# Kernel tuning notes

Measured on AMD Instinct MI355X. Metric: run time of the kernel, lower is better.

Reference implementation:

```python
import jax, jax.numpy as jnp
import numpy as np

N_NODES = 20000
NEG_SLOPE = 0.2
EPS = 1e-10


def _gat_reparam_layer(x, W, att_i, att_j, bias, src, dst, heads, c2):
    """GATConv (PyG-style, aggr='add') whose output encodes (mean, std) per head,
    followed by diag-Gaussian reparameterization with N(0,1) prior (eval mode:
    output = mean; ixz = KL(q||p) summed over channels, averaged over heads).
    x: [N, F]; W: [F, heads*c2]; att_i/att_j: [heads, c2]; bias: [heads*c2].
    c2 = 2 * out_channels (mean + std logits).
    Returns out [N, heads*(c2//2)], ixz [N]."""
    N = x.shape[0]
    h = (x @ W).reshape(N, heads, c2)                      # [N, H, 2C]
    h_i = h[dst]                                           # [E, H, 2C] target (x_i)
    h_j = h[src]                                           # [E, H, 2C] source (x_j)
    # attention logits: leaky_relu((x_i*att_i).sum + (x_j*att_j).sum)
    logits = jnp.sum(h_i * att_i, axis=-1) + jnp.sum(h_j * att_j, axis=-1)  # [E, H]
    logits = jax.nn.leaky_relu(logits, NEG_SLOPE)
    # segment softmax over incoming edges of each target node
    lmax = jax.ops.segment_max(logits, dst, num_segments=N)  # [N, H]
    ex = jnp.exp(logits - lmax[dst])                         # [E, H]
    denom = jax.ops.segment_sum(ex, dst, num_segments=N)     # [N, H]
    alpha = ex / denom[dst]                                  # [E, H]
    # weighted scatter-add aggregation
    msg = alpha[:, :, None] * h_j                            # [E, H, 2C]
    out = jax.ops.segment_sum(msg, dst, num_segments=N)      # [N, H, 2C]
    out = out + bias.reshape(1, heads, c2)
    # reparameterization: split per head into mean / std
    C = c2 // 2
    mean = out[..., :C]                                      # [N, H, C]
    std = jax.nn.softplus(out[..., C:]) + EPS                # [N, H, C]
    # KL(N(mean, std) || N(0, 1)) per element, sum over C, mean over heads
    kl = 0.5 * (std * std + mean * mean - 1.0) - jnp.log(std)
    ixz = kl.sum(-1).mean(-1)                                # [N]
    return mean.reshape(N, heads * C), ixz


def setup_inputs() -> dict:
    key = jax.random.key(0)
    ks = jax.random.split(key, 10)
    N, F1 = N_NODES, 256
    E = 320000
    H1, C1 = 8, 32    # conv1: latent_size//2 = 32 per head, doubled for (mean,std)
    H2, C2 = 1, 16    # conv2: num_classes = 16
    edge_index = jax.random.randint(ks[0], (2, E), 0, N, dtype=jnp.int32)
    s = 0.1
    return {
        "x": jax.random.normal(ks[1], (N, F1), jnp.float32),
        "edge_index": edge_index,
        "W1": jax.random.normal(ks[2], (F1, H1 * 2 * C1), jnp.float32) * s,
        "att_i1": jax.random.normal(ks[3], (H1, 2 * C1), jnp.float32) * s,
        "att_j1": jax.random.normal(ks[4], (H1, 2 * C1), jnp.float32) * s,
        "bias1": jax.random.normal(ks[5], (H1 * 2 * C1,), jnp.float32) * s,
        "W2": jax.random.normal(ks[6], (H1 * C1, H2 * 2 * C2), jnp.float32) * s,
        "att_i2": jax.random.normal(ks[7], (H2, 2 * C2), jnp.float32) * s,
        "att_j2": jax.random.normal(ks[8], (H2, 2 * C2), jnp.float32) * s,
        "bias2": jax.random.normal(ks[9], (H2 * 2 * C2,), jnp.float32) * s,
    }


def reference(x, edge_index, W1, att_i1, att_j1, bias1, W2, att_i2, att_j2, bias2):
    src, dst = edge_index[0], edge_index[1]
    # eval mode: dropout is identity, output = posterior mean (val_use_mean=True)
    h1, ixz1 = _gat_reparam_layer(x, W1, att_i1, att_j1, bias1, src, dst, heads=8, c2=64)
    h1 = jax.nn.elu(h1)
    h2, ixz2 = _gat_reparam_layer(h1, W2, att_i2, att_j2, bias2, src, dst, heads=1, c2=32)
    return h2
```

## Files before the change

kernel.cpp:

```cpp
#include <hip/hip_runtime.h>
#include <hip/hip_bf16.h>

#define NN 20000
#define EE 320000
#define NEG_SLOPE 0.2f
#define CAP1 96
#define BCAP 128

typedef unsigned short u16;
typedef short bf16x8 __attribute__((ext_vector_type(8)));
typedef unsigned short u16x8 __attribute__((ext_vector_type(8)));
typedef float f32x4 __attribute__((ext_vector_type(4)));

__device__ __forceinline__ u16 f2bf(float f) {
    unsigned u = __float_as_uint(f);
    return (u16)((u + 0x7FFFu + ((u >> 16) & 1u)) >> 16);
}
__device__ __forceinline__ float bf2f(u16 b) { return __uint_as_float(((unsigned)b) << 16); }

__device__ __forceinline__ void lds_fence() {
    asm volatile("s_waitcnt lgkmcnt(0)" ::: "memory");
}

__global__ __launch_bounds__(256) void init_pack(
    const float* __restrict__ W1, const float* __restrict__ atti1, const float* __restrict__ attj1,
    const float* __restrict__ W2, const float* __restrict__ atti2, const float* __restrict__ attj2,
    u16* __restrict__ Wp1, u16* __restrict__ Wp2, int* __restrict__ cursor)
{
    int b = blockIdx.x;
    if (b < 320) {
        int t = b*256 + threadIdx.x;
        int k = t & 255, j = t >> 8;
        float v = 0.f;
        if (j < 256) {
            v = W1[(size_t)k*512 + ((j>>5)*64 + (j&31))];
        } else if (j < 264) {
            int h = j - 256; float s = 0.f;
            for (int c = 0; c < 64; ++c) s += W1[(size_t)k*512 + h*64 + c] * atti1[h*64 + c];
            v = s;
        } else if (j < 272) {
            int h = j - 264; float s = 0.f;
            for (int c = 0; c < 64; ++c) s += W1[(size_t)k*512 + h*64 + c] * attj1[h*64 + c];
            v = s;
        }
        Wp1[t] = f2bf(v);
    } else if (b < 384) {
        int t = (b - 320)*256 + threadIdx.x;
        int k = t & 255, j = t >> 8;
        float v = 0.f;
        if (j < 16) {
            v = W2[(size_t)k*32 + j];
        } else if (j == 16) {
            float s = 0.f; for (int c = 0; c < 32; ++c) s += W2[(size_t)k*32 + c] * atti2[c]; v = s;
        } else if (j == 17) {
            float s = 0.f; for (int c = 0; c < 32; ++c) s += W2[(size_t)k*32 + c] * attj2[c]; v = s;
        }
        Wp2[t] = f2bf(v);
    } else {
        int i = (b - 384)*256 + threadIdx.x;
        if (i < NN) cursor[i] = 0;
    }
}

template<int NT, int EPI, int NWAVE, bool AF32>
__device__ __forceinline__ void gemm_body(
    int bx, int by, int tid,
    const void* __restrict__ Asrc, const u16* __restrict__ Bp, int M,
    u16* __restrict__ outB, float* __restrict__ outF,
    float* __restrict__ outAi, float* __restrict__ outAj)
{
    constexpr int BM = NWAVE*16;
    constexpr int BN = NT*16;
    __shared__ __align__(16) u16 lsA[BM*64];
    __shared__ __align__(16) u16 lsB[BN*64];

    const int w    = tid >> 6, lane = tid & 63;
    const int brow = by * BM, bcol = bx * BN;

    const int srow = tid >> 2;
    const int kseg = (tid & 3) * 16;
    const int aRow = min(brow + srow, M-1);
    const int s0   = kseg >> 3;
    const int wOff0 = srow*64 + ((s0    ) ^ (srow & 7))*8;
    const int wOff1 = srow*64 + ((s0 + 1) ^ (srow & 7))*8;

    const int frow = (w << 4) + (lane & 15);
    const int fkb  = lane >> 4;
    int aF[2], bF[2][NT];
    #pragma unroll
    for (int v = 0; v < 2; ++v) {
        aF[v] = frow*64 + (((v*4 + fkb) ^ (frow & 7)))*8;
        #pragma unroll
        for (int tt = 0; tt < NT; ++tt) {
            int col = tt*16 + (lane & 15);
            bF[v][tt] = col*64 + (((v*4 + fkb) ^ (col & 7)))*8;
        }
    }

    f32x4 acc[NT] = {};

    for (int ks = 0; ks < 4; ++ks) {
        const int k0 = ks*64;
        if constexpr (AF32) {
            const float* ap = (const float*)Asrc + (size_t)aRow*256 + k0 + kseg;
            float4 v0 = *(const float4*)(ap+0),  v1 = *(const float4*)(ap+4);
            float4 v2 = *(const float4*)(ap+8),  v3 = *(const float4*)(ap+12);
            u16x8 u0, u1;
            u0[0]=f2bf(v0.x); u0[1]=f2bf(v0.y); u0[2]=f2bf(v0.z); u0[3]=f2bf(v0.w);
            u0[4]=f2bf(v1.x); u0[5]=f2bf(v1.y); u0[6]=f2bf(v1.z); u0[7]=f2bf(v1.w);
            u1[0]=f2bf(v2.x); u1[1]=f2bf(v2.y); u1[2]=f2bf(v2.z); u1[3]=f2bf(v2.w);
            u1[4]=f2bf(v3.x); u1[5]=f2bf(v3.y); u1[6]=f2bf(v3.z); u1[7]=f2bf(v3.w);
            *(u16x8*)&lsA[wOff0] = u0;
            *(u16x8*)&lsA[wOff1] = u1;
        } else {
            const u16* ap = (const u16*)Asrc + (size_t)aRow*256 + k0 + kseg;
            *(u16x8*)&lsA[wOff0] = *(const u16x8*)(ap);
            *(u16x8*)&lsA[wOff1] = *(const u16x8*)(ap+8);
        }
        const u16* bp = Bp + (size_t)(bcol + srow)*256 + k0 + kseg;
        *(u16x8*)&lsB[wOff0] = *(const u16x8*)(bp);
        *(u16x8*)&lsB[wOff1] = *(const u16x8*)(bp+8);
        __syncthreads();
        #pragma unroll
        for (int v = 0; v < 2; ++v) {
            bf16x8 a = *(const bf16x8*)&lsA[aF[v]];
            #pragma unroll
            for (int tt = 0; tt < NT; ++tt) {
                bf16x8 b = *(const bf16x8*)&lsB[bF[v][tt]];
                acc[tt] = __builtin_amdgcn_mfma_f32_16x16x32_bf16(a, b, acc[tt], 0, 0, 0);
            }
        }
        __syncthreads();
    }

    #pragma unroll
    for (int tt = 0; tt < NT; ++tt) {
        int col = bcol + tt*16 + (lane & 15);
        #pragma unroll
        for (int r = 0; r < 4; ++r) {
            int row = brow + (w << 4) + ((lane >> 4) << 2) + r;
            if (row >= M) continue;
            float v = acc[tt][r];
            if constexpr (EPI == 1) {
                if      (col < 256) outB[(size_t)row*256 + col] = f2bf(v);
                else if (col < 264) outAi[(size_t)row*8 + (col - 256)] = v;
                else if (col < 272) outAj[(size_t)row*8 + (col - 264)] = v;
            } else {
                if      (col < 16)  outF[(size_t)row*16 + col] = v;
                else if (col == 16) outAi[row] = v;
                else if (col == 17) outAj[row] = v;
            }
        }
    }
}

#define G1_BLOCKS 1565
#define SC_BLOCKS 1250

__global__ __launch_bounds__(256) void fusedA(
    const float* __restrict__ x, const u16* __restrict__ Wp1,
    u16* __restrict__ h1m, float* __restrict__ ai1, float* __restrict__ aj1,
    const int* __restrict__ src, const int* __restrict__ dst,
    int* __restrict__ cursor, int* __restrict__ elist)
{
    int b = blockIdx.x;
    if (b < G1_BLOCKS) {
        gemm_body<4,1,4,true>(b % 5, b / 5, threadIdx.x, x, Wp1, NN, h1m, nullptr, ai1, aj1);
    } else {
        int e = (b - G1_BLOCKS)*256 + threadIdx.x;
        if (e < EE) {
            int d = dst[e];
            int pos = atomicAdd(&cursor[d], 1);
            if (pos < BCAP) elist[d*BCAP + pos] = src[e];
        }
    }
}

__global__ __launch_bounds__(128) void gemm2_k(
    const u16* __restrict__ h1b, const u16* __restrict__ Wp2, 
    float* __restrict__ h2m, float* __restrict__ ai2, float* __restrict__ aj2)
{
    gemm_body<2,2,2,false>(blockIdx.x, blockIdx.y, threadIdx.x, h1b, Wp2, NN, nullptr, h2m, ai2, aj2);
}

__global__ __launch_bounds__(256) void gat1_fused(
    const int* __restrict__ cursor, const int* __restrict__ elist,
    const float* __restrict__ ai, const float* __restrict__ aj,
    const u16* __restrict__ h1m, const float* __restrict__ bias,
    u16* __restrict__ h1b)
{
    __shared__ float s_w[4][CAP1*9];
    __shared__ int   s_src[4][CAP1];
    __shared__ float s_inv[4][8];

    const int wv = threadIdx.x >> 6, lane = threadIdx.x & 63;
    const int n = blockIdx.x*4 + wv;
    const int beg = n*BCAP;
    const int deg = min(cursor[n], BCAP);
    float* sw = s_w[wv];
    int*   ss = s_src[wv];

    float4 ai0 = *(const float4*)&ai[(size_t)n*8];
    float4 ai1 = *(const float4*)&ai[(size_t)n*8 + 4];
    float aiv[8] = {ai0.x,ai0.y,ai0.z,ai0.w,ai1.x,ai1.y,ai1.z,ai1.w};

    if (deg <= CAP1) {
        for (int e = lane; e < deg; e += 64) {
            int s = elist[beg + e];
            ss[e] = s;
            float4 a0 = *(const float4*)&aj[(size_t)s*8];
            float4 a1 = *(const float4*)&aj[(size_t)s*8 + 4];
            float av[8] = {a0.x,a0.y,a0.z,a0.w,a1.x,a1.y,a1.z,a1.w};
            #pragma unroll
            for (int h = 0; h < 8; ++h) {
                float l = aiv[h] + av[h];
                sw[e*9 + h] = (l >= 0.f) ? l : NEG_SLOPE * l;
            }
        }
        lds_fence();
        {
            int h = lane >> 3, sl = lane & 7;
            float mx = -INFINITY;
            for (int e = sl; e < deg; e += 8) mx = fmaxf(mx, sw[e*9 + h]);
            #pragma unroll
            for (int o = 1; o < 8; o <<= 1) mx = fmaxf(mx, __shfl_xor(mx, o, 64));
            float sm = 0.f;
            for (int e = sl; e < deg; e += 8) {
                float ex = __expf(sw[e*9 + h] - mx);
                sw[e*9 + h] = ex;
                sm += ex;
            }
            #pragma unroll
            for (int o = 1; o < 8; o <<= 1) sm += __shfl_xor(sm, o, 64);
            if (sl == 0) s_inv[wv][h] = (deg > 0) ? 1.f / sm : 0.f;
        }
        lds_fence();
        {
            int g = lane & 31, slot = lane >> 5, head = g >> 2;
            float inv = s_inv[wv][head];
            const u16* hb = h1m + (size_t)g*8;
            float acc[8] = {};
            int e = slot;
            for (; e + 6 < deg; e += 8) {
                int   i0 = ss[e],          i1 = ss[e+2],          i2 = ss[e+4],          i3 = ss[e+6];
                float w0 = sw[e*9+head],   w1 = sw[(e+2)*9+head], w2 = sw[(e+4)*9+head], w3 = sw[(e+6)*9+head];
                bf16x8 v0 = *(const bf16x8*)&hb[(size_t)i0*256];
                bf16x8 v1 = *(const bf16x8*)&hb[(size_t)i1*256];
                bf16x8 v2 = *(const bf16x8*)&hb[(size_t)i2*256];
                bf16x8 v3 = *(const bf16x8*)&hb[(size_t)i3*256];
                #pragma unroll
                for (int k = 0; k < 8; ++k) {
                    acc[k] += w0 * bf2f((u16)v0[k]);
                    acc[k] += w1 * bf2f((u16)v1[k]);
                    acc[k] += w2 * bf2f((u16)v2[k]);
                    acc[k] += w3 * bf2f((u16)v3[k]);
                }
            }
            for (; e < deg; e += 2) {
                float wgt = sw[e*9 + head];
                bf16x8 v = *(const bf16x8*)&hb[(size_t)ss[e]*256];
                #pragma unroll
                for (int k = 0; k < 8; ++k)
                    acc[k] += wgt * bf2f((u16)v[k]);
            }
            #pragma unroll
            for (int k = 0; k < 8; ++k) acc[k] += __shfl_xor(acc[k], 32, 64);
            if (lane < 32) {
                int cbase = (g & 3)*8;
                u16x8 o;
                #pragma unroll
                for (int k = 0; k < 8; ++k) {
                    float v = acc[k]*inv + bias[head*64 + cbase + k];
                    v = (v > 0.f) ? v : (__expf(v) - 1.0f);
                    o[k] = f2bf(v);
                }
                *(u16x8*)&h1b[(size_t)n*256 + g*8] = o;
            }
        }
    } else {
        for (int h = 0; h < 8; ++h) {
            float a_i = aiv[h];
            float mx = -INFINITY;
            for (int e = lane; e < deg; e += 64) {
                int s = elist[beg + e];
                float t = a_i + aj[(size_t)s*8 + h];
                t = (t >= 0.f) ? t : NEG_SLOPE * t;
                mx = fmaxf(mx, t);
            }
            #pragma unroll
            for (int o = 32; o > 0; o >>= 1) mx = fmaxf(mx, __shfl_xor(mx, o, 64));
            float sm = 0.f;
            for (int e = lane; e < deg; e += 64) {
                int s = elist[beg + e];
                float t = a_i + aj[(size_t)s*8 + h];
                t = (t >= 0.f) ? t : NEG_SLOPE * t;
                sm += __expf(t - mx);
            }
            #pragma unroll
            for (int o = 32; o > 0; o >>= 1) sm += __shfl_xor(sm, o, 64);
            float inv = (deg > 0) ? 1.f / sm : 0.f;
            int c = lane & 31, sl2 = lane >> 5;
            float a2 = 0.f;
            for (int e = sl2; e < deg; e += 2) {
                int s = elist[beg + e];
                float t = a_i + aj[(size_t)s*8 + h];
                t = (t >= 0.f) ? t : NEG_SLOPE * t;
                float wgt = __expf(t - mx);
                a2 += wgt * bf2f(h1m[(size_t)s*256 + h*32 + c]);
            }
            a2 += __shfl_xor(a2, 32, 64);
            if (lane < 32) {
                float v = a2*inv + bias[h*64 + c];
                v = (v > 0.f) ? v : (__expf(v) - 1.0f);
                h1b[(size_t)n*256 + h*32 + c] = f2bf(v);
            }
        }
    }
}

__global__ __launch_bounds__(256) void gat2_fused(
    const int* __restrict__ cursor, const int* __restrict__ elist,
    const float* __restrict__ ai, const float* __restrict__ aj,
    const float* __restrict__ h2m, const float* __restrict__ bias,
    float* __restrict__ outp)
{
    __shared__ float s_w2[4][64];
    __shared__ int   s_s2[4][64];

    const int wv = threadIdx.x >> 6, lane = threadIdx.x & 63;
    const int n = blockIdx.x*4 + wv;
    const int beg = n*BCAP;
    const int deg = min(cursor[n], BCAP);
    float a_i = ai[n];

    if (deg <= 64) {
        float l = -INFINITY; int s = 0;
        if (lane < deg) {
            s = elist[beg + lane];
            float t = a_i + aj[s];
            l = (t >= 0.f) ? t : NEG_SLOPE * t;
        }
        float mx = l;
        #pragma unroll
        for (int o = 32; o > 0; o >>= 1) mx = fmaxf(mx, __shfl_xor(mx, o, 64));
        float ex = (lane < deg) ? __expf(l - mx) : 0.f;
        float sm = ex;
        #pragma unroll
        for (int o = 32; o > 0; o >>= 1) sm += __shfl_xor(sm, o, 64);
        float inv = (deg > 0) ? 1.f / sm : 0.f;
        if (lane < deg) { s_w2[wv][lane] = ex; s_s2[wv][lane] = s; }
        lds_fence();
        int c4 = lane & 3, slot = lane >> 2;
        float4 acc = make_float4(0.f, 0.f, 0.f, 0.f);
        for (int e = slot; e < deg; e += 16) {
            float w = s_w2[wv][e];
            int sv = s_s2[wv][e];
            float4 v = *(const float4*)&h2m[(size_t)sv*16 + c4*4];
            acc.x += w*v.x; acc.y += w*v.y; acc.z += w*v.z; acc.w += w*v.w;
        }
        #pragma unroll
        for (int o = 4; o <= 32; o <<= 1) {
            acc.x += __shfl_xor(acc.x, o, 64);
            acc.y += __shfl_xor(acc.y, o, 64);
            acc.z += __shfl_xor(acc.z, o, 64);
            acc.w += __shfl_xor(acc.w, o, 64);
        }
        if (lane < 4) {
            const float4 b4 = *(const float4*)&bias[lane*4];
            float4 r = make_float4(acc.x*inv + b4.x, acc.y*inv + b4.y,
                                   acc.z*inv + b4.z, acc.w*inv + b4.w);
            *(float4*)&outp[(size_t)n*16 + lane*4] = r;
        }
    } else {
        float mx = -INFINITY;
        for (int e = lane; e < deg; e += 64) {
            int s2 = elist[beg + e];
            float t = a_i + aj[s2];
            t = (t >= 0.f) ? t : NEG_SLOPE * t;
            mx = fmaxf(mx, t);
        }
        #pragma unroll
        for (int o = 32; o > 0; o >>= 1) mx = fmaxf(mx, __shfl_xor(mx, o, 64));
        float sm = 0.f;
        for (int e = lane; e < deg; e += 64) {
            int s2 = elist[beg + e];
            float t = a_i + aj[s2];
            t = (t >= 0.f) ? t : NEG_SLOPE * t;
            sm += __expf(t - mx);
        }
        #pragma unroll
        for (int o = 32; o > 0; o >>= 1) sm += __shfl_xor(sm, o, 64);
        float inv = (deg > 0) ? 1.f / sm : 0.f;
        int c = lane & 15, e4 = lane >> 4;
        float acc = 0.f;
        for (int e = e4; e < deg; e += 4) {
            int s2 = elist[beg + e];
            float t = a_i + aj[s2];
            t = (t >= 0.f) ? t : NEG_SLOPE * t;
            float w = __expf(t - mx);
            acc += w * h2m[(size_t)s2*16 + c];
        }
        acc += __shfl_xor(acc, 16, 64);
        acc += __shfl_xor(acc, 32, 64);
        if (lane < 16) outp[(size_t)n*16 + lane] = acc*inv + bias[lane];
    }
}

static inline size_t al16(size_t x) { return (x + 15) & ~(size_t)15; }

extern "C" void kernel_launch(void* const* d_in, const int* in_sizes, int n_in,
                              void* d_out, int out_size, void* d_ws, size_t ws_size,
                              hipStream_t stream) {
    const float* x      = (const float*)d_in[0];
    const int*   ei     = (const int*)  d_in[1];
    const float* W1     = (const float*)d_in[2];
    const float* att_i1 = (const float*)d_in[3];
    const float* att_j1 = (const float*)d_in[4];
    const float* bias1  = (const float*)d_in[5];
    const float* W2     = (const float*)d_in[6];
    const float* att_i2 = (const float*)d_in[7];
    const float* att_j2 = (const float*)d_in[8];
    const float* bias2  = (const float*)d_in[9];
    float* out = (float*)d_out;

    const int N = NN, E = EE;
    const int* src = ei;
    const int* dst = ei + E;

    char* p = (char*)d_ws;
    #define CARVE(ty, name, elems) ty* name = (ty*)p; p += al16((size_t)(elems) * sizeof(ty));
    CARVE(u16,   Wp1,  320*256)
    CARVE(u16,   Wp2,  64*256)
    CARVE(u16,   h1m,  (size_t)N*256)
    CARVE(u16,   h1b,  (size_t)N*256)
    CARVE(float, ai1,  (size_t)N*8)
    CARVE(float, aj1,  (size_t)N*8)
    CARVE(float, h2m,  (size_t)N*16)
    CARVE(float, ai2,  N)
    CARVE(float, aj2,  N)
    CARVE(int,   cursor,   N)
    CARVE(int,   elist,    (size_t)N*BCAP)
    #undef CARVE

    const int BS = 256;
    const int NB = (N + 255) / 256;

    init_pack<<<384 + NB, BS, 0, stream>>>(W1, att_i1, att_j1, W2, att_i2, att_j2, Wp1, Wp2, cursor);

    fusedA<<<G1_BLOCKS + SC_BLOCKS, BS, 0, stream>>>(x, Wp1, h1m, ai1, aj1, src, dst, cursor, elist);

    gat1_fused<<<N/4, BS, 0, stream>>>(cursor, elist, ai1, aj1, h1m, bias1, h1b);

    {
        dim3 g(1, (N + 31) / 32);
        gemm2_k<<<g, 128, 0, stream>>>(h1b, Wp2, h2m, ai2, aj2);
    }

    gat2_fused<<<N/4, BS, 0, stream>>>(cursor, elist, ai2, aj2, h2m, bias2, out);
}
```

Measured before the change: 80.84 us.

## Fuse second-layer projection into GAT1 aggregation and pre-convert x to bf16

The second GEMM (h1 @ W2 plus attention projections) is folded into the first-layer aggregation kernel. Each wavefront keeps its node's ELU output in registers, takes dot products against a compact 18-column bf16 weight pack, and reduces with shuffles. This removes the h1b intermediate write and read and one kernel launch. Separately, x is converted to bf16 in the init kernel, so the main GEMM reads bf16 directly at the cost of an extra full pass over x.

```diff
diff --git a/kernel.cpp b/kernel.cpp
--- a/kernel.cpp
+++ b/kernel.cpp
@@ -22,13 +22,18 @@
     asm volatile("s_waitcnt lgkmcnt(0)" ::: "memory");
 }
 
+#define IB_W1 320
+#define IB_W2 338
+#define IB_CU 417
+#define IB_XB 2917
 __global__ __launch_bounds__(256) void init_pack(
+    const float* __restrict__ x,
     const float* __restrict__ W1, const float* __restrict__ atti1, const float* __restrict__ attj1,
     const float* __restrict__ W2, const float* __restrict__ atti2, const float* __restrict__ attj2,
-    u16* __restrict__ Wp1, u16* __restrict__ Wp2, int* __restrict__ cursor)
+    u16* __restrict__ Wp1, u16* __restrict__ Wp2, int* __restrict__ cursor, u16* __restrict__ xb)
 {
     int b = blockIdx.x;
-    if (b < 320) {
+    if (b < IB_W1) {
         int t = b*256 + threadIdx.x;
         int k = t & 255, j = t >> 8;
         float v = 0.f;
@@ -44,38 +49,42 @@
             v = s;
         }
         Wp1[t] = f2bf(v);
-    } else if (b < 384) {
-        int t = (b - 320)*256 + threadIdx.x;
-        int k = t & 255, j = t >> 8;
-        float v = 0.f;
+    } else if (b < IB_W2) {
+        int j = b - IB_W1;
+        int k = threadIdx.x;
+        float v;
         if (j < 16) {
             v = W2[(size_t)k*32 + j];
         } else if (j == 16) {
             float s = 0.f; for (int c = 0; c < 32; ++c) s += W2[(size_t)k*32 + c] * atti2[c]; v = s;
-        } else if (j == 17) {
+        } else {
             float s = 0.f; for (int c = 0; c < 32; ++c) s += W2[(size_t)k*32 + c] * attj2[c]; v = s;
         }
-        Wp2[t] = f2bf(v);
+        Wp2[j*256 + k] = f2bf(v);
+    } else if (b < IB_CU) {
+        int i = (b - IB_W2)*256 + threadIdx.x;
+        if (i < NN) cursor[i] = 0;
     } else {
-        int i = (b - 384)*256 + threadIdx.x;
-        if (i < NN) cursor[i] = 0;
-    }
-}
-
-template<int NT, int EPI, int NWAVE, bool AF32>
+        size_t gb = ((size_t)(b - IB_CU)*256 + threadIdx.x) * 8;
+        float4 v0 = *(const float4*)&x[gb];
+        float4 v1 = *(const float4*)&x[gb + 4];
+        u16x8 u;
+        u[0]=f2bf(v0.x); u[1]=f2bf(v0.y); u[2]=f2bf(v0.z); u[3]=f2bf(v0.w);
+        u[4]=f2bf(v1.x); u[5]=f2bf(v1.y); u[6]=f2bf(v1.z); u[7]=f2bf(v1.w);
+        *(u16x8*)&xb[gb] = u;
+    }
+}
+
 __device__ __forceinline__ void gemm_body(
     int bx, int by, int tid,
-    const void* __restrict__ Asrc, const u16* __restrict__ Bp, int M,
-    u16* __restrict__ outB, float* __restrict__ outF,
-    float* __restrict__ outAi, float* __restrict__ outAj)
+    const u16* __restrict__ Ab, const u16* __restrict__ Bp, int M,
+    u16* __restrict__ outB, float* __restrict__ outAi, float* __restrict__ outAj)
 {
-    constexpr int BM = NWAVE*16;
-    constexpr int BN = NT*16;
-    __shared__ __align__(16) u16 lsA[BM*64];
-    __shared__ __align__(16) u16 lsB[BN*64];
+    __shared__ __align__(16) u16 lsA[64*64];
+    __shared__ __align__(16) u16 lsB[64*64];
 
     const int w    = tid >> 6, lane = tid & 63;
-    const int brow = by * BM, bcol = bx * BN;
+    const int brow = by * 64, bcol = bx * 64;
 
     const int srow = tid >> 2;
     const int kseg = (tid & 3) * 16;
@@ -86,37 +95,24 @@
 
     const int frow = (w << 4) + (lane & 15);
     const int fkb  = lane >> 4;
-    int aF[2], bF[2][NT];
+    int aF[2], bF[2][4];
     #pragma unroll
     for (int v = 0; v < 2; ++v) {
         aF[v] = frow*64 + (((v*4 + fkb) ^ (frow & 7)))*8;
         #pragma unroll
-        for (int tt = 0; tt < NT; ++tt) {
+        for (int tt = 0; tt < 4; ++tt) {
             int col = tt*16 + (lane & 15);
             bF[v][tt] = col*64 + (((v*4 + fkb) ^ (col & 7)))*8;
         }
     }
 
-    f32x4 acc[NT] = {};
+    f32x4 acc[4] = {};
 
     for (int ks = 0; ks < 4; ++ks) {
         const int k0 = ks*64;
-        if constexpr (AF32) {
-            const float* ap = (const float*)Asrc + (size_t)aRow*256 + k0 + kseg;
-            float4 v0 = *(const float4*)(ap+0),  v1 = *(const float4*)(ap+4);
-            float4 v2 = *(const float4*)(ap+8),  v3 = *(const float4*)(ap+12);
-            u16x8 u0, u1;
-            u0[0]=f2bf(v0.x); u0[1]=f2bf(v0.y); u0[2]=f2bf(v0.z); u0[3]=f2bf(v0.w);
-            u0[4]=f2bf(v1.x); u0[5]=f2bf(v1.y); u0[6]=f2bf(v1.z); u0[7]=f2bf(v1.w);
-            u1[0]=f2bf(v2.x); u1[1]=f2bf(v2.y); u1[2]=f2bf(v2.z); u1[3]=f2bf(v2.w);
-            u1[4]=f2bf(v3.x); u1[5]=f2bf(v3.y); u1[6]=f2bf(v3.z); u1[7]=f2bf(v3.w);
-            *(u16x8*)&lsA[wOff0] = u0;
-            *(u16x8*)&lsA[wOff1] = u1;
-        } else {
-            const u16* ap = (const u16*)Asrc + (size_t)aRow*256 + k0 + kseg;
-            *(u16x8*)&lsA[wOff0] = *(const u16x8*)(ap);
-            *(u16x8*)&lsA[wOff1] = *(const u16x8*)(ap+8);
-        }
+        const u16* ap = Ab + (size_t)aRow*256 + k0 + kseg;
+        *(u16x8*)&lsA[wOff0] = *(const u16x8*)(ap);
+        *(u16x8*)&lsA[wOff1] = *(const u16x8*)(ap+8);
         const u16* bp = Bp + (size_t)(bcol + srow)*256 + k0 + kseg;
         *(u16x8*)&lsB[wOff0] = *(const u16x8*)(bp);
         *(u16x8*)&lsB[wOff1] = *(const u16x8*)(bp+8);
@@ -125,7 +121,7 @@
         for (int v = 0; v < 2; ++v) {
             bf16x8 a = *(const bf16x8*)&lsA[aF[v]];
             #pragma unroll
-            for (int tt = 0; tt < NT; ++tt) {
+            for (int tt = 0; tt < 4; ++tt) {
                 bf16x8 b = *(const bf16x8*)&lsB[bF[v][tt]];
                 acc[tt] = __builtin_amdgcn_mfma_f32_16x16x32_bf16(a, b, acc[tt], 0, 0, 0);
             }
@@ -134,22 +130,16 @@
     }
 
     #pragma unroll
-    for (int tt = 0; tt < NT; ++tt) {
+    for (int tt = 0; tt < 4; ++tt) {
         int col = bcol + tt*16 + (lane & 15);
         #pragma unroll
         for (int r = 0; r < 4; ++r) {
             int row = brow + (w << 4) + ((lane >> 4) << 2) + r;
             if (row >= M) continue;
             float v = acc[tt][r];
-            if constexpr (EPI == 1) {
-                if      (col < 256) outB[(size_t)row*256 + col] = f2bf(v);
-                else if (col < 264) outAi[(size_t)row*8 + (col - 256)] = v;
-                else if (col < 272) outAj[(size_t)row*8 + (col - 264)] = v;
-            } else {
-                if      (col < 16)  outF[(size_t)row*16 + col] = v;
-                else if (col == 16) outAi[row] = v;
-                else if (col == 17) outAj[row] = v;
-            }
+            if      (col < 256) outB[(size_t)row*256 + col] = f2bf(v);
+            else if (col < 264) outAi[(size_t)row*8 + (col - 256)] = v;
+            else if (col < 272) outAj[(size_t)row*8 + (col - 264)] = v;
         }
     }
 }
@@ -158,14 +148,14 @@
 #define SC_BLOCKS 1250
 
 __global__ __launch_bounds__(256) void fusedA(
-    const float* __restrict__ x, const u16* __restrict__ Wp1,
+    const u16* __restrict__ xb, const u16* __restrict__ Wp1,
     u16* __restrict__ h1m, float* __restrict__ ai1, float* __restrict__ aj1,
     const int* __restrict__ src, const int* __restrict__ dst,
     int* __restrict__ cursor, int* __restrict__ elist)
 {
     int b = blockIdx.x;
     if (b < G1_BLOCKS) {
-        gemm_body<4,1,4,true>(b % 5, b / 5, threadIdx.x, x, Wp1, NN, h1m, nullptr, ai1, aj1);
+        gemm_body(b % 5, b / 5, threadIdx.x, xb, Wp1, NN, h1m, ai1, aj1);
     } else {
         int e = (b - G1_BLOCKS)*256 + threadIdx.x;
         if (e < EE) {
@@ -176,18 +166,12 @@
     }
 }
 
-__global__ __launch_bounds__(128) void gemm2_k(
-    const u16* __restrict__ h1b, const u16* __restrict__ Wp2, 
-    float* __restrict__ h2m, float* __restrict__ ai2, float* __restrict__ aj2)
-{
-    gemm_body<2,2,2,false>(blockIdx.x, blockIdx.y, threadIdx.x, h1b, Wp2, NN, nullptr, h2m, ai2, aj2);
-}
-
-__global__ __launch_bounds__(256) void gat1_fused(
+__global__ __launch_bounds__(256) void gat1g2(
     const int* __restrict__ cursor, const int* __restrict__ elist,
     const float* __restrict__ ai, const float* __restrict__ aj,
     const u16* __restrict__ h1m, const float* __restrict__ bias,
-    u16* __restrict__ h1b)
+    const u16* __restrict__ Wp2,
+    float* __restrict__ h2m, float* __restrict__ ai2, float* __restrict__ aj2)
 {
     __shared__ float s_w[4][CAP1*9];
     __shared__ int   s_src[4][CAP1];
@@ -201,8 +185,11 @@
     int*   ss = s_src[wv];
 
     float4 ai0 = *(const float4*)&ai[(size_t)n*8];
-    float4 ai1 = *(const float4*)&ai[(size_t)n*8 + 4];
-    float aiv[8] = {ai0.x,ai0.y,ai0.z,ai0.w,ai1.x,ai1.y,ai1.z,ai1.w};
+    float4 ai1v = *(const float4*)&ai[(size_t)n*8 + 4];
+    float aiv[8] = {ai0.x,ai0.y,ai0.z,ai0.w,ai1v.x,ai1v.y,ai1v.z,ai1v.w};
+
+    const int g = lane & 31, head = g >> 2, cbase = (g & 3)*8;
+    float v[8];
 
     if (deg <= CAP1) {
         for (int e = lane; e < deg; e += 64) {
@@ -236,7 +223,7 @@
         }
         lds_fence();
         {
-            int g = lane & 31, slot = lane >> 5, head = g >> 2;
+            int slot = lane >> 5;
             float inv = s_inv[wv][head];
             const u16* hb = h1m + (size_t)g*8;
             float acc[8] = {};
@@ -258,26 +245,21 @@
             }
             for (; e < deg; e += 2) {
                 float wgt = sw[e*9 + head];
-                bf16x8 v = *(const bf16x8*)&hb[(size_t)ss[e]*256];
+                bf16x8 vx = *(const bf16x8*)&hb[(size_t)ss[e]*256];
                 #pragma unroll
                 for (int k = 0; k < 8; ++k)
-                    acc[k] += wgt * bf2f((u16)v[k]);
+                    acc[k] += wgt * bf2f((u16)vx[k]);
             }
             #pragma unroll
             for (int k = 0; k < 8; ++k) acc[k] += __shfl_xor(acc[k], 32, 64);
-            if (lane < 32) {
-                int cbase = (g & 3)*8;
-                u16x8 o;
-                #pragma unroll
-                for (int k = 0; k < 8; ++k) {
-                    float v = acc[k]*inv + bias[head*64 + cbase + k];
-                    v = (v > 0.f) ? v : (__expf(v) - 1.0f);
-                    o[k] = f2bf(v);
-                }
-                *(u16x8*)&h1b[(size_t)n*256 + g*8] = o;
+            #pragma unroll
+            for (int k = 0; k < 8; ++k) {
+                float t = acc[k]*inv + bias[head*64 + cbase + k];
+                v[k] = (t > 0.f) ? t : (__expf(t) - 1.0f);
             }
         }
     } else {
+        float* sh = sw;
         for (int h = 0; h < 8; ++h) {
             float a_i = aiv[h];
             float mx = -INFINITY;
@@ -310,10 +292,39 @@
             }
             a2 += __shfl_xor(a2, 32, 64);
             if (lane < 32) {
-                float v = a2*inv + bias[h*64 + c];
-                v = (v > 0.f) ? v : (__expf(v) - 1.0f);
-                h1b[(size_t)n*256 + h*32 + c] = f2bf(v);
-            }
+                float t = a2*inv + bias[h*64 + c];
+                sh[h*32 + c] = (t > 0.f) ? t : (__expf(t) - 1.0f);
+            }
+        }
+        lds_fence();
+        #pragma unroll
+        for (int k = 0; k < 8; ++k) v[k] = sh[g*8 + k];
+    }
+
+    {
+        int jbase = (lane >> 5) * 9;
+        float p[9];
+        #pragma unroll
+        for (int jj = 0; jj < 9; ++jj) {
+            u16x8 wr = *(const u16x8*)&Wp2[(size_t)(jbase + jj)*256 + g*8];
+            float s = 0.f;
+            #pragma unroll
+            for (int k = 0; k < 8; ++k) s += v[k] * bf2f((u16)wr[k]);
+            p[jj] = s;
+        }
+        #pragma unroll
+        for (int o = 1; o < 32; o <<= 1) {
+            #pragma unroll
+            for (int jj = 0; jj < 9; ++jj) p[jj] += __shfl_xor(p[jj], o, 64);
+        }
+        float outv = p[0];
+        #pragma unroll
+        for (int jj = 1; jj < 9; ++jj) if (g == jj) outv = p[jj];
+        if (g < 9) {
+            int j = jbase + g;
+            if      (j < 16)  h2m[(size_t)n*16 + j] = outv;
+            else if (j == 16) ai2[n] = outv;
+            else if (j == 17) aj2[n] = outv;
         }
     }
 }
@@ -355,8 +366,8 @@
         for (int e = slot; e < deg; e += 16) {
             float w = s_w2[wv][e];
             int sv = s_s2[wv][e];
-            float4 v = *(const float4*)&h2m[(size_t)sv*16 + c4*4];
-            acc.x += w*v.x; acc.y += w*v.y; acc.z += w*v.z; acc.w += w*v.w;
+            float4 vv = *(const float4*)&h2m[(size_t)sv*16 + c4*4];
+            acc.x += w*vv.x; acc.y += w*vv.y; acc.z += w*vv.z; acc.w += w*vv.w;
         }
         #pragma unroll
         for (int o = 4; o <= 32; o <<= 1) {
@@ -430,9 +441,9 @@
     char* p = (char*)d_ws;
     #define CARVE(ty, name, elems) ty* name = (ty*)p; p += al16((size_t)(elems) * sizeof(ty));
     CARVE(u16,   Wp1,  320*256)
-    CARVE(u16,   Wp2,  64*256)
+    CARVE(u16,   Wp2,  18*256)
+    CARVE(u16,   xb,   (size_t)N*256)
     CARVE(u16,   h1m,  (size_t)N*256)
-    CARVE(u16,   h1b,  (size_t)N*256)
     CARVE(float, ai1,  (size_t)N*8)
     CARVE(float, aj1,  (size_t)N*8)
     CARVE(float, h2m,  (size_t)N*16)
@@ -443,18 +454,15 @@
     #undef CARVE
 
     const int BS = 256;
-    const int NB = (N + 255) / 256;
-
-    init_pack<<<384 + NB, BS, 0, stream>>>(W1, att_i1, att_j1, W2, att_i2, att_j2, Wp1, Wp2, cursor);
-
-    fusedA<<<G1_BLOCKS + SC_BLOCKS, BS, 0, stream>>>(x, Wp1, h1m, ai1, aj1, src, dst, cursor, elist);
-
-    gat1_fused<<<N/4, BS, 0, stream>>>(cursor, elist, ai1, aj1, h1m, bias1, h1b);
-
-    {
-        dim3 g(1, (N + 31) / 32);
-        gemm2_k<<<g, 128, 0, stream>>>(h1b, Wp2, h2m, ai2, aj2);
-    }
+
+    init_pack<<<IB_XB, BS, 0, stream>>>(x, W1, att_i1, att_j1, W2, att_i2, att_j2,
+                                        Wp1, Wp2, cursor, xb);
+
+    fusedA<<<G1_BLOCKS + SC_BLOCKS, BS, 0, stream>>>(xb, Wp1, h1m, ai1, aj1,
+                                                     src, dst, cursor, elist);
+
+    gat1g2<<<N/4, BS, 0, stream>>>(cursor, elist, ai1, aj1, h1m, bias1, Wp2,
+                                   h2m, ai2, aj2);
 
     gat2_fused<<<N/4, BS, 0, stream>>>(cursor, elist, ai2, aj2, h2m, bias2, out);
 }
```

Result: no change. 79.93 us (-1.1%).
